# Kernel optimization log

Measured on AMD Instinct MI355X. Metric: run time of the kernel, lower is better.

Reference implementation:

```python
import jax, jax.numpy as jnp
import numpy as np

N_OBJ, N_ROOM, N_ATTR = 20000, 500, 2000
IN_FEATS, H = 300, 512
E_OO, E_RO, E_AO = 640000, 50000, 100000
B = 8


def setup_inputs() -> dict:
    key = jax.random.key(0)
    ks = jax.random.split(key, 16)
    s = 0.05
    inp = {
        'frames': jax.random.normal(ks[0], (B, H), jnp.float32),
        'feat_object': jax.random.normal(ks[1], (N_OBJ, IN_FEATS), jnp.float32),
        'feat_room': jax.random.normal(ks[2], (N_ROOM, IN_FEATS), jnp.float32),
        'feat_attr': jax.random.normal(ks[3], (N_ATTR, IN_FEATS), jnp.float32),
        'W1_interacts': jax.random.normal(ks[4], (IN_FEATS, H), jnp.float32) * s,
        'b1_interacts': jnp.zeros((H,), jnp.float32),
        'W1_behave': jax.random.normal(ks[5], (IN_FEATS, H), jnp.float32) * s,
        'b1_behave': jnp.zeros((H,), jnp.float32),
        'W2_interacts': jax.random.normal(ks[6], (H, H), jnp.float32) * s,
        'b2_interacts': jnp.zeros((H,), jnp.float32),
        'src_oo': jax.random.randint(ks[7], (E_OO,), 0, N_OBJ, jnp.int32),
        'dst_oo': jax.random.randint(ks[8], (E_OO,), 0, N_OBJ, jnp.int32),
        'src_ro': jax.random.randint(ks[9], (E_RO,), 0, N_ROOM, jnp.int32),
        'dst_ro': jax.random.randint(ks[10], (E_RO,), 0, N_OBJ, jnp.int32),
        'src_ao': jax.random.randint(ks[11], (E_AO,), 0, N_ATTR, jnp.int32),
        'dst_ao': jax.random.randint(ks[12], (E_AO,), 0, N_OBJ, jnp.int32),
    }
    return inp


def _graph_conv(feat_src, src, dst, n_dst, W, b, relu):
    # DGL GraphConv, norm='both': D_dst^{-1/2} A D_src^{-1/2} X W + b
    n_src = feat_src.shape[0]
    ones_e = jnp.ones(src.shape[0], feat_src.dtype)
    deg_out = jax.ops.segment_sum(ones_e, src, num_segments=n_src)
    norm_src = jnp.clip(deg_out, 1.0, None) ** -0.5
    msg = (feat_src * norm_src[:, None])[src]          # [E, F] gather
    agg = jax.ops.segment_sum(msg, dst, num_segments=n_dst)  # scatter-sum
    deg_in = jax.ops.segment_sum(ones_e, dst, num_segments=n_dst)
    norm_dst = jnp.clip(deg_in, 1.0, None) ** -0.5
    out = (agg * norm_dst[:, None]) @ W + b
    return jax.nn.relu(out) if relu else out


def reference(frames, feat_object, feat_room, feat_attr,
              W1_interacts, b1_interacts, W1_behave, b1_behave,
              W2_interacts, b2_interacts,
              src_oo, dst_oo, src_ro, dst_ro, src_ao, dst_ao):
    # conv1: three relations, all dst='object'; HeteroGraphConv mean aggregate
    h_oo = _graph_conv(feat_object, src_oo, dst_oo, N_OBJ, W1_interacts, b1_interacts, True)
    h_ro = _graph_conv(feat_room, src_ro, dst_ro, N_OBJ, W1_interacts, b1_interacts, True)
    h_ao = _graph_conv(feat_attr, src_ao, dst_ao, N_OBJ, W1_behave, b1_behave, True)
    h_obj = (h_oo + h_ro + h_ao) / 3.0
    # conv2: only object->object (room not in conv1 output dict); mean over 1 rel
    h2 = _graph_conv(h_obj, src_oo, dst_oo, N_OBJ, W2_interacts, b2_interacts, False)
    # HETAttention=True: repeat over frames batch dim
    x = jnp.broadcast_to(h2[None], (frames.shape[0], N_OBJ, H))
    return x
```

## Files before the change

### kernel.cpp

```cpp
#include <hip/hip_runtime.h>

#define N_OBJ  20000
#define N_ROOM 500
#define N_ATTR 2000
#define IN_F   300
#define HDIM   512
#define E_OO   640000
#define E_RO   50000
#define E_AO   100000
#define BATCH  8

typedef __attribute__((ext_vector_type(8))) __bf16 bf16x8;
typedef __attribute__((ext_vector_type(4))) float  f32x4;

__device__ inline unsigned short f2bf_rn(float x)
{
    unsigned u = __float_as_uint(x);
    unsigned r = (u + 0x7fffu + ((u >> 16) & 1u)) >> 16;
    return (unsigned short)r;
}
__device__ inline float bf2f(unsigned short h)
{
    return __uint_as_float(((unsigned)h) << 16);
}

__global__ void count_edges(const int* __restrict__ src_oo, const int* __restrict__ dst_oo,
                            const int* __restrict__ src_ro, const int* __restrict__ dst_ro,
                            const int* __restrict__ src_ao, const int* __restrict__ dst_ao,
                            int* cnt_src_oo, int* cnt_src_ro, int* cnt_src_ao,
                            int* cnt_dst_oo, int* cnt_dst_ro, int* cnt_dst_ao)
{
    int e = blockIdx.x * blockDim.x + threadIdx.x;
    const int total = E_OO + E_RO + E_AO;
    if (e >= total) return;
    if (e < E_OO) {
        atomicAdd(&cnt_src_oo[src_oo[e]], 1);
        atomicAdd(&cnt_dst_oo[dst_oo[e]], 1);
    } else if (e < E_OO + E_RO) {
        int i = e - E_OO;
        atomicAdd(&cnt_src_ro[src_ro[i]], 1);
        atomicAdd(&cnt_dst_ro[dst_ro[i]], 1);
    } else {
        int i = e - E_OO - E_RO;
        atomicAdd(&cnt_src_ao[src_ao[i]], 1);
        atomicAdd(&cnt_dst_ao[dst_ao[i]], 1);
    }
}

__global__ __launch_bounds__(1024)
void scan3(const int* c0, const int* c1, const int* c2,
           int* r0, int* r1, int* r2,
           int* u0, int* u1, int* u2)
{
    const int n = N_OBJ;
    const int* cnt = (blockIdx.x == 0) ? c0 : (blockIdx.x == 1 ? c1 : c2);
    int* rp  = (blockIdx.x == 0) ? r0 : (blockIdx.x == 1 ? r1 : r2);
    int* cur = (blockIdx.x == 0) ? u0 : (blockIdx.x == 1 ? u1 : u2);

    __shared__ int part[1024];
    int t  = threadIdx.x;
    int lo = t * 20;
    int hi = lo + 20 < n ? lo + 20 : n;

    int local = 0;
    for (int i = lo; i < hi; ++i) local += cnt[i];
    part[t] = local;
    __syncthreads();
    for (int off = 1; off < 1024; off <<= 1) {
        int v = (t >= off) ? part[t - off] : 0;
        __syncthreads();
        part[t] += v;
        __syncthreads();
    }
    int run = part[t] - local;
    for (int i = lo; i < hi; ++i) {
        rp[i]  = run;
        cur[i] = run;
        run += cnt[i];
    }
    if (t == 1023) rp[n] = part[1023];
}

__global__ void norms6(const int* c0, const int* c1, const int* c2,
                       const int* c3, const int* c4, const int* c5,
                       float* n0, float* n1, float* n2,
                       float* n3, float* n4, float* n5,
                       int s0, int s1, int s2, int s3, int s4, int s5)
{
    const int* c; float* o; int n;
    switch (blockIdx.y) {
        case 0:  c = c0; o = n0; n = s0; break;
        case 1:  c = c1; o = n1; n = s1; break;
        case 2:  c = c2; o = n2; n = s2; break;
        case 3:  c = c3; o = n3; n = s3; break;
        case 4:  c = c4; o = n4; n = s4; break;
        default: c = c5; o = n5; n = s5; break;
    }
    int i = blockIdx.x * blockDim.x + threadIdx.x;
    if (i < n) {
        int d = c[i];
        if (d < 1) d = 1;
        o[i] = 1.0f / sqrtf((float)d);
    }
}

__global__ void fill_edges(const int* __restrict__ src_oo, const int* __restrict__ dst_oo,
                           const int* __restrict__ src_ro, const int* __restrict__ dst_ro,
                           const int* __restrict__ src_ao, const int* __restrict__ dst_ao,
                           int* cur_oo, int* cur_ro, int* cur_ao,
                           int* col_oo, int* col_ro, int* col_ao)
{
    int e = blockIdx.x * blockDim.x + threadIdx.x;
    const int total = E_OO + E_RO + E_AO;
    if (e >= total) return;
    if (e < E_OO) {
        int pos = atomicAdd(&cur_oo[dst_oo[e]], 1);
        col_oo[pos] = src_oo[e];
    } else if (e < E_OO + E_RO) {
        int i = e - E_OO;
        int pos = atomicAdd(&cur_ro[dst_ro[i]], 1);
        col_ro[pos] = src_ro[i];
    } else {
        int i = e - E_OO - E_RO;
        int pos = atomicAdd(&cur_ao[dst_ao[i]], 1);
        col_ao[pos] = src_ao[i];
    }
}

__global__ void pack_w(const float* __restrict__ W, int K, int Kp,
                       unsigned short* __restrict__ Wp)
{
    int Keff = 3 * Kp;
    int idx = blockIdx.x * 256 + threadIdx.x;
    if (idx >= HDIM * Keff) return;
    int n  = idx / Keff;
    int kp = idx - n * Keff;
    int term = (kp >= 2 * Kp) ? 2 : (kp >= Kp ? 1 : 0);
    int ks = kp - term * Kp;
    float v = (ks < K) ? W[(size_t)ks * HDIM + n] : 0.0f;
    unsigned short h = f2bf_rn(v);
    unsigned short out = (term == 1) ? f2bf_rn(v - bf2f(h)) : h;
    Wp[idx] = out;
}

__global__ __launch_bounds__(256)
void agg_csr_split(const float* __restrict__ feat, int F, int Fp,
                   const int* __restrict__ rp, const int* __restrict__ col,
                   const float* __restrict__ nsrc, const float* __restrict__ ndst,
                   float scale,
                   unsigned short* __restrict__ hi, unsigned short* __restrict__ lo)
{
    int d = blockIdx.x;
    int t = threadIdx.x;
    int a = rp[d], b = rp[d + 1];
    int f2 = 256 + t;
    bool has2  = (f2 < Fp);
    bool real2 = (f2 < F);
    float acc0 = 0.f, acc1 = 0.f;
    for (int j = a; j < b; ++j) {
        int s = col[j];
        float ns = nsrc[s] * scale;
        acc0 += feat[(size_t)s * F + t] * ns;
        if (real2) acc1 += feat[(size_t)s * F + f2] * ns;
    }
    float nd = ndst[d];
    acc0 *= nd;
    acc1 = real2 ? acc1 * nd : 0.f;

    size_t o0 = (size_t)d * Fp + t;
    unsigned short h0 = f2bf_rn(acc0);
    hi[o0] = h0;
    lo[o0] = f2bf_rn(acc0 - bf2f(h0));
    if (has2) {
        size_t o1 = (size_t)d * Fp + f2;
        unsigned short h1 = f2bf_rn(acc1);
        hi[o1] = h1;
        lo[o1] = f2bf_rn(acc1 - bf2f(h1));
    }
}

template<int EPI>
__global__ __launch_bounds__(256)
void gemm_mfma(const unsigned short* __restrict__ Ah,
               const unsigned short* __restrict__ Al,
               const unsigned short* __restrict__ Wp,
               const float* __restrict__ bias,
               float* __restrict__ C,
               int M, int Kp)
{
    const int LDT = 40;
    __shared__ unsigned short As[128 * LDT];
    __shared__ unsigned short Bs[128 * LDT];

    int tid  = threadIdx.x;
    int lane = tid & 63;
    int wave = tid >> 6;
    int wm = (wave & 1) * 64;
    int wn = (wave >> 1) * 64;
    int m0 = blockIdx.x * 128;
    int n0 = blockIdx.y * 128;
    int Keff = 3 * Kp;
    int rw = lane & 15;
    int q  = lane >> 4;

    f32x4 acc[4][4];
#pragma unroll
    for (int i = 0; i < 4; ++i)
#pragma unroll
        for (int j = 0; j < 4; ++j) acc[i][j] = (f32x4)0.0f;

    for (int k0 = 0; k0 < Keff; k0 += 32) {
        int term = (k0 >= 2 * Kp) ? 2 : (k0 >= Kp ? 1 : 0);
        int kb = k0 - ((term == 2) ? 2 * Kp : (term == 1 ? Kp : 0));
        const unsigned short* Asrc = (term == 2) ? Al : Ah;
#pragma unroll
        for (int h = 0; h < 2; ++h) {
            int idx = tid + h * 256;
            int m = idx >> 2, kc = (idx & 3) * 8;
            int gm = m0 + m;
            uint4 v = make_uint4(0u, 0u, 0u, 0u);
            if (gm < M) v = *(const uint4*)(Asrc + (size_t)gm * Kp + kb + kc);
            *(uint4*)&As[m * LDT + kc] = v;
        }
#pragma unroll
        for (int h = 0; h < 2; ++h) {
            int idx = tid + h * 256;
            int nn = idx >> 2, kc = (idx & 3) * 8;
            uint4 v = *(const uint4*)(Wp + (size_t)(n0 + nn) * Keff + k0 + kc);
            *(uint4*)&Bs[nn * LDT + kc] = v;
        }
        __syncthreads();

        bf16x8 af[4], bfr[4];
#pragma unroll
        for (int i = 0; i < 4; ++i) {
            af[i]  = __builtin_bit_cast(bf16x8, *(const uint4*)&As[(wm + i * 16 + rw) * LDT + q * 8]);
            bfr[i] = __builtin_bit_cast(bf16x8, *(const uint4*)&Bs[(wn + i * 16 + rw) * LDT + q * 8]);
        }
#pragma unroll
        for (int i = 0; i < 4; ++i)
#pragma unroll
            for (int j = 0; j < 4; ++j)
                acc[i][j] = __builtin_amdgcn_mfma_f32_16x16x32_bf16(af[i], bfr[j], acc[i][j], 0, 0, 0);
        __syncthreads();
    }

    const size_t slice = (size_t)N_OBJ * HDIM;
#pragma unroll
    for (int j = 0; j < 4; ++j) {
        int n = n0 + wn + j * 16 + rw;
        float bv = bias[n];
#pragma unroll
        for (int i = 0; i < 4; ++i) {
#pragma unroll
            for (int r = 0; r < 4; ++r) {
                int m = m0 + wm + i * 16 + q * 4 + r;
                if (m < M) {
                    float v = acc[i][j][r] + bv;
                    size_t o = (size_t)m * HDIM + n;
                    if (EPI == 0)      C[o] = fmaxf(v, 0.f);
                    else if (EPI == 1) C[o] += fmaxf(v, 0.f);
                    else if (EPI == 2) {
#pragma unroll
                        for (int c = 0; c < BATCH; ++c) C[c * slice + o] = v;
                    } else             C[o] = v;
                }
            }
        }
    }
}

__global__ void bcast8(const float4* __restrict__ src, float4* __restrict__ dst)
{
    const long long slice4 = (long long)N_OBJ * HDIM / 4;
    long long i = (long long)blockIdx.x * blockDim.x + threadIdx.x;
    float4 v = src[i];
#pragma unroll
    for (int c = 1; c < BATCH; ++c)
        dst[c * slice4 + i] = v;
}

extern "C" void kernel_launch(void* const* d_in, const int* in_sizes, int n_in,
                              void* d_out, int out_size, void* d_ws, size_t ws_size,
                              hipStream_t stream)
{
    const float* feat_object = (const float*)d_in[1];
    const float* feat_room   = (const float*)d_in[2];
    const float* feat_attr   = (const float*)d_in[3];
    const float* W1i = (const float*)d_in[4];
    const float* b1i = (const float*)d_in[5];
    const float* W1b = (const float*)d_in[6];
    const float* b1b = (const float*)d_in[7];
    const float* W2  = (const float*)d_in[8];
    const float* b2  = (const float*)d_in[9];
    const int* src_oo = (const int*)d_in[10];
    const int* dst_oo = (const int*)d_in[11];
    const int* src_ro = (const int*)d_in[12];
    const int* dst_ro = (const int*)d_in[13];
    const int* src_ao = (const int*)d_in[14];
    const int* dst_ao = (const int*)d_in[15];
    float* out = (float*)d_out;

    const size_t slice = (size_t)N_OBJ * HDIM;
    const int KP1 = 320;
    const int KP2 = 512;

    const size_t NEED = 130u * 1024u * 1024u;
    bool use_ws = (ws_size >= NEED);
    char* base = use_ws ? (char*)d_ws : (char*)(out + slice);
    size_t off = 0;
    auto alloc = [&](size_t bytes) -> void* {
        void* p = base + off;
        off += (bytes + 255) & ~(size_t)255;
        return p;
    };

    float* n_src_oo = (float*)alloc(N_OBJ  * 4);
    float* n_src_ro = (float*)alloc(N_ROOM * 4);
    float* n_src_ao = (float*)alloc(N_ATTR * 4);
    float* n_dst_oo = (float*)alloc(N_OBJ * 4);
    float* n_dst_ro = (float*)alloc(N_OBJ * 4);
    float* n_dst_ao = (float*)alloc(N_OBJ * 4);

    const int CNT_TOTAL = N_OBJ + 512 + 2048 + 3 * N_OBJ;
    int* cnt_blk    = (int*)alloc((size_t)CNT_TOTAL * 4);
    int* cnt_src_oo = cnt_blk;
    int* cnt_src_ro = cnt_src_oo + N_OBJ;
    int* cnt_src_ao = cnt_src_ro + 512;
    int* cnt_dst_oo = cnt_src_ao + 2048;
    int* cnt_dst_ro = cnt_dst_oo + N_OBJ;
    int* cnt_dst_ao = cnt_dst_ro + N_OBJ;

    int* rp_oo  = (int*)alloc((N_OBJ + 1) * 4);
    int* rp_ro  = (int*)alloc((N_OBJ + 1) * 4);
    int* rp_ao  = (int*)alloc((N_OBJ + 1) * 4);
    int* cur_oo = (int*)alloc(N_OBJ * 4);
    int* cur_ro = (int*)alloc(N_OBJ * 4);
    int* cur_ao = (int*)alloc(N_OBJ * 4);
    int* col_oo = (int*)alloc((size_t)E_OO * 4);
    int* col_ro = (int*)alloc((size_t)E_RO * 4);
    int* col_ao = (int*)alloc((size_t)E_AO * 4);

    unsigned short* Ah1 = (unsigned short*)alloc((size_t)N_OBJ * KP1 * 2);
    unsigned short* Al1 = (unsigned short*)alloc((size_t)N_OBJ * KP1 * 2);
    unsigned short* Ah2 = (unsigned short*)alloc((size_t)N_OBJ * KP2 * 2);
    unsigned short* Al2 = (unsigned short*)alloc((size_t)N_OBJ * KP2 * 2);
    unsigned short* Wp1i = (unsigned short*)alloc((size_t)HDIM * 3 * KP1 * 2);
    unsigned short* Wp1b = (unsigned short*)alloc((size_t)HDIM * 3 * KP1 * 2);
    unsigned short* Wp2  = (unsigned short*)alloc((size_t)HDIM * 3 * KP2 * 2);
    float* h_sum = (float*)alloc(slice * 4);

    hipMemsetAsync(cnt_blk, 0, (size_t)CNT_TOTAL * 4, stream);
    const int TOTAL_E = E_OO + E_RO + E_AO;
    int egrid = (TOTAL_E + 255) / 256;
    count_edges<<<egrid, 256, 0, stream>>>(src_oo, dst_oo, src_ro, dst_ro, src_ao, dst_ao,
                                           cnt_src_oo, cnt_src_ro, cnt_src_ao,
                                           cnt_dst_oo, cnt_dst_ro, cnt_dst_ao);
    scan3<<<3, 1024, 0, stream>>>(cnt_dst_oo, cnt_dst_ro, cnt_dst_ao,
                                  rp_oo, rp_ro, rp_ao, cur_oo, cur_ro, cur_ao);
    norms6<<<dim3((N_OBJ + 255) / 256, 6), 256, 0, stream>>>(
        cnt_src_oo, cnt_src_ro, cnt_src_ao, cnt_dst_oo, cnt_dst_ro, cnt_dst_ao,
        n_src_oo, n_src_ro, n_src_ao, n_dst_oo, n_dst_ro, n_dst_ao,
        N_OBJ, N_ROOM, N_ATTR, N_OBJ, N_OBJ, N_OBJ);
    fill_edges<<<egrid, 256, 0, stream>>>(src_oo, dst_oo, src_ro, dst_ro, src_ao, dst_ao,
                                          cur_oo, cur_ro, cur_ao, col_oo, col_ro, col_ao);

    {
        int e1 = HDIM * 3 * KP1, e2 = HDIM * 3 * KP2;
        pack_w<<<(e1 + 255) / 256, 256, 0, stream>>>(W1i, IN_F, KP1, Wp1i);
        pack_w<<<(e1 + 255) / 256, 256, 0, stream>>>(W1b, IN_F, KP1, Wp1b);
        pack_w<<<(e2 + 255) / 256, 256, 0, stream>>>(W2, HDIM, KP2, Wp2);
    }

    dim3 ggrid((N_OBJ + 127) / 128, HDIM / 128);

    agg_csr_split<<<N_OBJ, 256, 0, stream>>>(feat_object, IN_F, KP1, rp_oo, col_oo,
                                             n_src_oo, n_dst_oo, 1.0f, Ah1, Al1);
    gemm_mfma<0><<<ggrid, 256, 0, stream>>>(Ah1, Al1, Wp1i, b1i, h_sum, N_OBJ, KP1);

    agg_csr_split<<<N_OBJ, 256, 0, stream>>>(feat_room, IN_F, KP1, rp_ro, col_ro,
                                             n_src_ro, n_dst_ro, 1.0f, Ah1, Al1);
    gemm_mfma<1><<<ggrid, 256, 0, stream>>>(Ah1, Al1, Wp1i, b1i, h_sum, N_OBJ, KP1);

    agg_csr_split<<<N_OBJ, 256, 0, stream>>>(feat_attr, IN_F, KP1, rp_ao, col_ao,
                                             n_src_ao, n_dst_ao, 1.0f, Ah1, Al1);
    gemm_mfma<1><<<ggrid, 256, 0, stream>>>(Ah1, Al1, Wp1b, b1b, h_sum, N_OBJ, KP1);

    agg_csr_split<<<N_OBJ, 256, 0, stream>>>(h_sum, HDIM, KP2, rp_oo, col_oo,
                                             n_src_oo, n_dst_oo, 1.0f / 3.0f, Ah2, Al2);
    if (use_ws) {
        gemm_mfma<2><<<ggrid, 256, 0, stream>>>(Ah2, Al2, Wp2, b2, out, N_OBJ, KP2);
    } else {
        gemm_mfma<3><<<ggrid, 256, 0, stream>>>(Ah2, Al2, Wp2, b2, out, N_OBJ, KP2);
        const long long slice4 = (long long)slice / 4;
        bcast8<<<(unsigned)(slice4 / 256), 256, 0, stream>>>((const float4*)out, (float4*)out);
    }
}
```

Baseline: 1.181 ms.

## Fuse three conv1 GEMMs, vectorize aggregation, prefetch GEMM tiles via registers

Aggregation now gives one wave per destination node and uses float4 loads and packed bf16 hi/lo stores, instead of a 256-thread block per node with scalar accesses. The three conv1 relation GEMMs become a single kernel that loops over all three relations, applying bias and ReLU and summing in registers. This removes the read-modify-write passes over h_sum and two kernel launches. The GEMM also prefetches the next K tile into registers while MFMAs run on the current one. In exchange, the three aggregated relation buffers must all stay resident, the workspace requirement rises, and register pressure grows from the extra accumulators.

Result: slower. 1.429 ms (+21.0%).

```diff
diff --git a/kernel.cpp b/kernel.cpp
--- a/kernel.cpp
+++ b/kernel.cpp
@@ -143,51 +143,73 @@
     Wp[idx] = out;
 }
 
+template<int F, int FP>
 __global__ __launch_bounds__(256)
-void agg_csr_split(const float* __restrict__ feat, int F, int Fp,
-                   const int* __restrict__ rp, const int* __restrict__ col,
-                   const float* __restrict__ nsrc, const float* __restrict__ ndst,
-                   float scale,
-                   unsigned short* __restrict__ hi, unsigned short* __restrict__ lo)
-{
-    int d = blockIdx.x;
-    int t = threadIdx.x;
+void agg_split_v4(const float* __restrict__ feat,
+                  const int* __restrict__ rp, const int* __restrict__ col,
+                  const float* __restrict__ nsrc, const float* __restrict__ ndst,
+                  float scale,
+                  unsigned short* __restrict__ hi, unsigned short* __restrict__ lo)
+{
+    constexpr int S  = F / 4;
+    constexpr int SP = FP / 4;
+    int wave = threadIdx.x >> 6, lane = threadIdx.x & 63;
+    int d = blockIdx.x * 4 + wave;
+    if (d >= N_OBJ) return;
     int a = rp[d], b = rp[d + 1];
-    int f2 = 256 + t;
-    bool has2  = (f2 < Fp);
-    bool real2 = (f2 < F);
-    float acc0 = 0.f, acc1 = 0.f;
+    bool has0 = (lane < S);
+    bool has1 = (lane + 64 < S);
+    f32x4 acc0 = (f32x4)0.0f, acc1 = (f32x4)0.0f;
     for (int j = a; j < b; ++j) {
         int s = col[j];
         float ns = nsrc[s] * scale;
-        acc0 += feat[(size_t)s * F + t] * ns;
-        if (real2) acc1 += feat[(size_t)s * F + f2] * ns;
+        const float* row = feat + (size_t)s * F;
+        if (has0) acc0 += (*(const f32x4*)(row + lane * 4)) * ns;
+        if (has1) acc1 += (*(const f32x4*)(row + (lane + 64) * 4)) * ns;
     }
     float nd = ndst[d];
-    acc0 *= nd;
-    acc1 = real2 ? acc1 * nd : 0.f;
-
-    size_t o0 = (size_t)d * Fp + t;
-    unsigned short h0 = f2bf_rn(acc0);
-    hi[o0] = h0;
-    lo[o0] = f2bf_rn(acc0 - bf2f(h0));
-    if (has2) {
-        size_t o1 = (size_t)d * Fp + f2;
-        unsigned short h1 = f2bf_rn(acc1);
-        hi[o1] = h1;
-        lo[o1] = f2bf_rn(acc1 - bf2f(h1));
-    }
-}
-
-template<int EPI>
+    acc0 *= nd; acc1 *= nd;
+
+    size_t rb = (size_t)d * FP;
+    if (lane < SP) {
+        f32x4 v = has0 ? acc0 : (f32x4)0.0f;
+        ushort4 h, l;
+        h.x = f2bf_rn(v.x); l.x = f2bf_rn(v.x - bf2f(h.x));
+        h.y = f2bf_rn(v.y); l.y = f2bf_rn(v.y - bf2f(h.y));
+        h.z = f2bf_rn(v.z); l.z = f2bf_rn(v.z - bf2f(h.z));
+        h.w = f2bf_rn(v.w); l.w = f2bf_rn(v.w - bf2f(h.w));
+        *(ushort4*)(hi + rb + lane * 4) = h;
+        *(ushort4*)(lo + rb + lane * 4) = l;
+    }
+    if (lane + 64 < SP) {
+        f32x4 v = has1 ? acc1 : (f32x4)0.0f;
+        ushort4 h, l;
+        h.x = f2bf_rn(v.x); l.x = f2bf_rn(v.x - bf2f(h.x));
+        h.y = f2bf_rn(v.y); l.y = f2bf_rn(v.y - bf2f(h.y));
+        h.z = f2bf_rn(v.z); l.z = f2bf_rn(v.z - bf2f(h.z));
+        h.w = f2bf_rn(v.w); l.w = f2bf_rn(v.w - bf2f(h.w));
+        *(ushort4*)(hi + rb + (lane + 64) * 4) = h;
+        *(ushort4*)(lo + rb + (lane + 64) * 4) = l;
+    }
+}
+
+template<int KP, int NREL, int EPI>
 __global__ __launch_bounds__(256)
-void gemm_mfma(const unsigned short* __restrict__ Ah,
-               const unsigned short* __restrict__ Al,
-               const unsigned short* __restrict__ Wp,
-               const float* __restrict__ bias,
-               float* __restrict__ C,
-               int M, int Kp)
-{
+void gemm_pipe(const unsigned short* __restrict__ AhA,
+               const unsigned short* __restrict__ AlA,
+               const unsigned short* __restrict__ AhB,
+               const unsigned short* __restrict__ AlB,
+               const unsigned short* __restrict__ AhC,
+               const unsigned short* __restrict__ AlC,
+               const unsigned short* __restrict__ WpA,
+               const unsigned short* __restrict__ WpB,
+               const float* __restrict__ biasA,
+               const float* __restrict__ biasB,
+               float* __restrict__ C, int M)
+{
+    constexpr int KEFF = 3 * KP;
+    constexpr int NIT  = KEFF / 32;
+    constexpr int TOT  = NREL * NIT;
     const int LDT = 40;
     __shared__ unsigned short As[128 * LDT];
     __shared__ unsigned short Bs[128 * LDT];
@@ -199,37 +221,44 @@
     int wn = (wave >> 1) * 64;
     int m0 = blockIdx.x * 128;
     int n0 = blockIdx.y * 128;
-    int Keff = 3 * Kp;
     int rw = lane & 15;
     int q  = lane >> 4;
 
-    f32x4 acc[4][4];
+    int sm = tid >> 2;
+    int sk = (tid & 3) * 8;
+
+    int gm0 = m0 + sm;      if (gm0 >= M) gm0 = M - 1;
+    int gm1 = m0 + 64 + sm; if (gm1 >= M) gm1 = M - 1;
+
+    f32x4 acc[4][4], sum[4][4];
 #pragma unroll
     for (int i = 0; i < 4; ++i)
 #pragma unroll
-        for (int j = 0; j < 4; ++j) acc[i][j] = (f32x4)0.0f;
-
-    for (int k0 = 0; k0 < Keff; k0 += 32) {
-        int term = (k0 >= 2 * Kp) ? 2 : (k0 >= Kp ? 1 : 0);
-        int kb = k0 - ((term == 2) ? 2 * Kp : (term == 1 ? Kp : 0));
-        const unsigned short* Asrc = (term == 2) ? Al : Ah;
-#pragma unroll
-        for (int h = 0; h < 2; ++h) {
-            int idx = tid + h * 256;
-            int m = idx >> 2, kc = (idx & 3) * 8;
-            int gm = m0 + m;
-            uint4 v = make_uint4(0u, 0u, 0u, 0u);
-            if (gm < M) v = *(const uint4*)(Asrc + (size_t)gm * Kp + kb + kc);
-            *(uint4*)&As[m * LDT + kc] = v;
-        }
-#pragma unroll
-        for (int h = 0; h < 2; ++h) {
-            int idx = tid + h * 256;
-            int nn = idx >> 2, kc = (idx & 3) * 8;
-            uint4 v = *(const uint4*)(Wp + (size_t)(n0 + nn) * Keff + k0 + kc);
-            *(uint4*)&Bs[nn * LDT + kc] = v;
-        }
+        for (int j = 0; j < 4; ++j) { acc[i][j] = (f32x4)0.0f; sum[i][j] = (f32x4)0.0f; }
+
+    uint4 ra0, ra1, rb0, rb1;
+    auto load_tile = [&](int g) {
+        int r  = g / NIT;
+        int kk = (g - r * NIT) * 32;
+        const unsigned short* Ah = (NREL == 1 || r == 0) ? AhA : (r == 1 ? AhB : AhC);
+        const unsigned short* Al = (NREL == 1 || r == 0) ? AlA : (r == 1 ? AlB : AlC);
+        const unsigned short* Wp = (NREL == 3 && r == 2) ? WpB : WpA;
+        const unsigned short* Asrc = (kk >= 2 * KP) ? Al : Ah;
+        int kb = kk - ((kk >= 2 * KP) ? 2 * KP : (kk >= KP ? KP : 0));
+        ra0 = *(const uint4*)(Asrc + (size_t)gm0 * KP + kb + sk);
+        ra1 = *(const uint4*)(Asrc + (size_t)gm1 * KP + kb + sk);
+        rb0 = *(const uint4*)(Wp + (size_t)(n0 + sm) * KEFF + kk + sk);
+        rb1 = *(const uint4*)(Wp + (size_t)(n0 + 64 + sm) * KEFF + kk + sk);
+    };
+
+    load_tile(0);
+    for (int g = 0; g < TOT; ++g) {
+        *(uint4*)&As[sm * LDT + sk]        = ra0;
+        *(uint4*)&As[(64 + sm) * LDT + sk] = ra1;
+        *(uint4*)&Bs[sm * LDT + sk]        = rb0;
+        *(uint4*)&Bs[(64 + sm) * LDT + sk] = rb1;
         __syncthreads();
+        if (g + 1 < TOT) load_tile(g + 1);
 
         bf16x8 af[4], bfr[4];
 #pragma unroll
@@ -242,6 +271,23 @@
 #pragma unroll
             for (int j = 0; j < 4; ++j)
                 acc[i][j] = __builtin_amdgcn_mfma_f32_16x16x32_bf16(af[i], bfr[j], acc[i][j], 0, 0, 0);
+
+        if (NREL == 3 && ((g + 1) % NIT == 0)) {
+            int r = g / NIT;
+            const float* bias = (r == 2) ? biasB : biasA;
+#pragma unroll
+            for (int j = 0; j < 4; ++j) {
+                float bv = bias[n0 + wn + j * 16 + rw];
+#pragma unroll
+                for (int i = 0; i < 4; ++i) {
+#pragma unroll
+                    for (int t = 0; t < 4; ++t) {
+                        sum[i][j][t] += fmaxf(acc[i][j][t] + bv, 0.0f);
+                        acc[i][j][t] = 0.0f;
+                    }
+                }
+            }
+        }
         __syncthreads();
     }
 
@@ -249,21 +295,21 @@
 #pragma unroll
     for (int j = 0; j < 4; ++j) {
         int n = n0 + wn + j * 16 + rw;
-        float bv = bias[n];
+        float bv = (NREL == 1) ? biasA[n] : 0.0f;
 #pragma unroll
         for (int i = 0; i < 4; ++i) {
 #pragma unroll
-            for (int r = 0; r < 4; ++r) {
-                int m = m0 + wm + i * 16 + q * 4 + r;
+            for (int t = 0; t < 4; ++t) {
+                int m = m0 + wm + i * 16 + q * 4 + t;
                 if (m < M) {
-                    float v = acc[i][j][r] + bv;
+                    float v = (NREL == 3) ? sum[i][j][t] : acc[i][j][t] + bv;
                     size_t o = (size_t)m * HDIM + n;
-                    if (EPI == 0)      C[o] = fmaxf(v, 0.f);
-                    else if (EPI == 1) C[o] += fmaxf(v, 0.f);
-                    else if (EPI == 2) {
+                    if (EPI == 2) {
 #pragma unroll
                         for (int c = 0; c < BATCH; ++c) C[c * slice + o] = v;
-                    } else             C[o] = v;
+                    } else {
+                        C[o] = v;
+                    }
                 }
             }
         }
@@ -305,7 +351,7 @@
     const int KP1 = 320;
     const int KP2 = 512;
 
-    const size_t NEED = 130u * 1024u * 1024u;
+    const size_t NEED = 200u * 1024u * 1024u;
     bool use_ws = (ws_size >= NEED);
     char* base = use_ws ? (char*)d_ws : (char*)(out + slice);
     size_t off = 0;
@@ -341,8 +387,12 @@
     int* col_ro = (int*)alloc((size_t)E_RO * 4);
     int* col_ao = (int*)alloc((size_t)E_AO * 4);
 
-    unsigned short* Ah1 = (unsigned short*)alloc((size_t)N_OBJ * KP1 * 2);
-    unsigned short* Al1 = (unsigned short*)alloc((size_t)N_OBJ * KP1 * 2);
+    unsigned short* AhO = (unsigned short*)alloc((size_t)N_OBJ * KP1 * 2);
+    unsigned short* AlO = (unsigned short*)alloc((size_t)N_OBJ * KP1 * 2);
+    unsigned short* AhR = (unsigned short*)alloc((size_t)N_OBJ * KP1 * 2);
+    unsigned short* AlR = (unsigned short*)alloc((size_t)N_OBJ * KP1 * 2);
+    unsigned short* AhAt = (unsigned short*)alloc((size_t)N_OBJ * KP1 * 2);
+    unsigned short* AlAt = (unsigned short*)alloc((size_t)N_OBJ * KP1 * 2);
     unsigned short* Ah2 = (unsigned short*)alloc((size_t)N_OBJ * KP2 * 2);
     unsigned short* Al2 = (unsigned short*)alloc((size_t)N_OBJ * KP2 * 2);
     unsigned short* Wp1i = (unsigned short*)alloc((size_t)HDIM * 3 * KP1 * 2);
@@ -372,26 +422,27 @@
         pack_w<<<(e2 + 255) / 256, 256, 0, stream>>>(W2, HDIM, KP2, Wp2);
     }
 
+    int agrid = (N_OBJ + 3) / 4;
+    agg_split_v4<IN_F, 320><<<agrid, 256, 0, stream>>>(feat_object, rp_oo, col_oo,
+                                                       n_src_oo, n_dst_oo, 1.0f, AhO, AlO);
+    agg_split_v4<IN_F, 320><<<agrid, 256, 0, stream>>>(feat_room, rp_ro, col_ro,
+                                                       n_src_ro, n_dst_ro, 1.0f, AhR, AlR);
+    agg_split_v4<IN_F, 320><<<agrid, 256, 0, stream>>>(feat_attr, rp_ao, col_ao,
+                                                       n_src_ao, n_dst_ao, 1.0f, AhAt, AlAt);
+
     dim3 ggrid((N_OBJ + 127) / 128, HDIM / 128);
-
-    agg_csr_split<<<N_OBJ, 256, 0, stream>>>(feat_object, IN_F, KP1, rp_oo, col_oo,
-                                             n_src_oo, n_dst_oo, 1.0f, Ah1, Al1);
-    gemm_mfma<0><<<ggrid, 256, 0, stream>>>(Ah1, Al1, Wp1i, b1i, h_sum, N_OBJ, KP1);
-
-    agg_csr_split<<<N_OBJ, 256, 0, stream>>>(feat_room, IN_F, KP1, rp_ro, col_ro,
-                                             n_src_ro, n_dst_ro, 1.0f, Ah1, Al1);
-    gemm_mfma<1><<<ggrid, 256, 0, stream>>>(Ah1, Al1, Wp1i, b1i, h_sum, N_OBJ, KP1);
-
-    agg_csr_split<<<N_OBJ, 256, 0, stream>>>(feat_attr, IN_F, KP1, rp_ao, col_ao,
-                                             n_src_ao, n_dst_ao, 1.0f, Ah1, Al1);
-    gemm_mfma<1><<<ggrid, 256, 0, stream>>>(Ah1, Al1, Wp1b, b1b, h_sum, N_OBJ, KP1);
-
-    agg_csr_split<<<N_OBJ, 256, 0, stream>>>(h_sum, HDIM, KP2, rp_oo, col_oo,
-                                             n_src_oo, n_dst_oo, 1.0f / 3.0f, Ah2, Al2);
+    gemm_pipe<KP1, 3, 0><<<ggrid, 256, 0, stream>>>(
+        AhO, AlO, AhR, AlR, AhAt, AlAt, Wp1i, Wp1b, b1i, b1b, h_sum, N_OBJ);
+
+    agg_split_v4<HDIM, HDIM><<<agrid, 256, 0, stream>>>(h_sum, rp_oo, col_oo,
+                                                        n_src_oo, n_dst_oo, 1.0f / 3.0f,
+                                                        Ah2, Al2);
     if (use_ws) {
-        gemm_mfma<2><<<ggrid, 256, 0, stream>>>(Ah2, Al2, Wp2, b2, out, N_OBJ, KP2);
+        gemm_pipe<KP2, 1, 2><<<ggrid, 256, 0, stream>>>(
+            Ah2, Al2, Ah2, Al2, Ah2, Al2, Wp2, Wp2, b2, b2, out, N_OBJ);
     } else {
-        gemm_mfma<3><<<ggrid, 256, 0, stream>>>(Ah2, Al2, Wp2, b2, out, N_OBJ, KP2);
+        gemm_pipe<KP2, 1, 3><<<ggrid, 256, 0, stream>>>(
+            Ah2, Al2, Ah2, Al2, Ah2, Al2, Wp2, Wp2, b2, b2, out, N_OBJ);
         const long long slice4 = (long long)slice / 4;
         bcast8<<<(unsigned)(slice4 / 256), 256, 0, stream>>>((const float4*)out, (float4*)out);
     }
```
